# Optimization experiments

Hardware: AMD Instinct MI355X
Metric: run time of the kernel (lower is better)

Reference implementation:

```python
import jax, jax.numpy as jnp
import numpy as np

B, K = 16, 50
IN_CH, N_CLASSES, N_ANCH = 256, 80, 3
STRIDE, FSIZE, IGNORE_THRE = 8, 76, 0.7
N_CH = 5 + N_CLASSES
ANCHORS = np.array([[10,13],[16,30],[33,23],[30,61],[62,45],[59,119],[116,90],[156,198],[373,326]], np.float32)
ALL_GRID = ANCHORS / STRIDE            # all 9 anchors in grid units
ANCH_MASK = np.array([0, 1, 2])        # layer_no = 2
MASKED = ALL_GRID[ANCH_MASK]           # (3,2) anchors used by this head


def setup_inputs():
    key = jax.random.key(0)
    k1, k2, k3, k4, k5, k6 = jax.random.split(key, 6)
    xin = jax.random.normal(k1, (B, IN_CH, FSIZE, FSIZE), jnp.float32)
    cls = jax.random.randint(k2, (B, K), 0, N_CLASSES).astype(jnp.float32)
    xy = jax.random.uniform(k3, (B, K, 2), minval=0.05, maxval=0.95)
    wh = jax.random.uniform(k4, (B, K, 2), minval=0.02, maxval=0.30)
    labels = jnp.concatenate([cls[..., None], xy, wh], -1)   # (B,K,5) [cls,xc,yc,w,h]
    oc = N_ANCH * N_CH
    conv_w = jax.random.normal(k5, (oc, IN_CH), jnp.float32) * 0.01
    conv_b = jax.random.normal(k6, (oc,), jnp.float32) * 0.01
    return {"xin": xin, "labels": labels, "conv_w": conv_w, "conv_b": conv_b}


def _yolo(xin, conv_w, conv_b, labels):
    f, C = FSIZE, N_CLASSES
    # 1x1 conv == channel matmul
    raw = jnp.einsum('bchw,oc->bohw', xin, conv_w) + conv_b[None, :, None, None]
    raw = raw.reshape(B, N_ANCH, N_CH, f, f).transpose(0, 1, 3, 4, 2)  # (B,A,f,f,85)
    # sigmoid on x,y,obj,cls; w,h stay raw
    out = jnp.concatenate([jax.nn.sigmoid(raw[..., :2]), raw[..., 2:4], jax.nn.sigmoid(raw[..., 4:])], -1)

    grid = jnp.arange(f, dtype=jnp.float32)
    mw = jnp.asarray(MASKED[:, 0]); mh = jnp.asarray(MASKED[:, 1])
    px = out[..., 0] + grid[None, None, None, :]
    py = out[..., 1] + grid[None, None, :, None]
    pw = jnp.exp(out[..., 2]) * mw[None, :, None, None]
    ph = jnp.exp(out[..., 3]) * mh[None, :, None, None]
    pred = jax.lax.stop_gradient(jnp.stack([px, py, pw, ph], -1))  # detached, like torch .data

    labels = jax.lax.stop_gradient(labels)
    valid = labels.sum(-1) > 0                  # (B,K) padding rows are all-zero
    tx = labels[..., 1] * f; ty = labels[..., 2] * f
    tw = labels[..., 3] * f; th = labels[..., 4] * f
    ii = tx.astype(jnp.int32); jj = ty.astype(jnp.int32)

    # anchor matching: IoU of [0,0,w,h] truth vs [0,0,aw,ah] ref anchors (corners at origin)
    aw = jnp.asarray(ALL_GRID[:, 0]); ah = jnp.asarray(ALL_GRID[:, 1])
    inter_a = jnp.minimum(tw[..., None], aw) * jnp.minimum(th[..., None], ah)  # (B,K,9)
    iou_a = inter_a / (tw[..., None] * th[..., None] + aw * ah - inter_a)
    best_n_all = jnp.argmax(iou_a, -1)
    best_n = best_n_all % 3
    best_mask = (best_n_all == ANCH_MASK[0]) | (best_n_all == ANCH_MASK[1]) | (best_n_all == ANCH_MASK[2])

    # pred-vs-truth IoU in cxcywh form (xyxy=False)
    pa = pred.reshape(B, -1, 4)                 # (B, A*f*f, 4)
    tb = jnp.stack([tx, ty, tw, th], -1)        # (B, K, 4)
    tl = jnp.maximum(pa[:, :, None, :2] - pa[:, :, None, 2:] * 0.5, tb[:, None, :, :2] - tb[:, None, :, 2:] * 0.5)
    br = jnp.minimum(pa[:, :, None, :2] + pa[:, :, None, 2:] * 0.5, tb[:, None, :, :2] + tb[:, None, :, 2:] * 0.5)
    en = jnp.all(tl < br, -1)
    inter = jnp.prod(br - tl, -1) * en
    area_p = pa[..., 2] * pa[..., 3]; area_t = tb[..., 2] * tb[..., 3]
    iou_p = inter / (area_p[:, :, None] + area_t[:, None, :] - inter)
    iou_p = jnp.where(valid[:, None, :], iou_p, 0.0)
    ignore = (iou_p.max(-1) > IGNORE_THRE).reshape(B, N_ANCH, f, f)
    obj_mask = 1.0 - ignore.astype(jnp.float32)

    # scatter positive targets; non-selected rows routed out-of-bounds and dropped
    sel = valid & best_mask
    bb = jnp.where(sel, jnp.arange(B)[:, None], B)
    obj_mask = obj_mask.at[bb, best_n, jj, ii].set(1.0, mode='drop')
    tgt_mask = jnp.zeros((B, N_ANCH, f, f, 4 + C)).at[bb, best_n, jj, ii].set(1.0, mode='drop')
    scale = jnp.sqrt(2.0 - tw * th / (f * f))
    tgt_scale = jnp.zeros((B, N_ANCH, f, f, 2)).at[bb, best_n, jj, ii].set(
        jnp.broadcast_to(scale[..., None], (B, K, 2)), mode='drop')
    tvals = jnp.concatenate([
        (tx - ii)[..., None], (ty - jj)[..., None],
        jnp.log(tw / mw[best_n] + 1e-16)[..., None],
        jnp.log(th / mh[best_n] + 1e-16)[..., None],
        jnp.ones((B, K, 1), jnp.float32),
        jax.nn.one_hot(labels[..., 0].astype(jnp.int32), C)], -1)  # (B,K,85)
    target = jnp.zeros((B, N_ANCH, f, f, N_CH)).at[bb, best_n, jj, ii].set(tvals, mode='drop')

    oxy = out[..., :2] * tgt_mask[..., :2]
    owh = out[..., 2:4] * tgt_mask[..., 2:4] * tgt_scale
    oob = out[..., 4] * obj_mask
    ocl = out[..., 5:] * tgt_mask[..., 4:]
    txy = target[..., :2] * tgt_mask[..., :2]
    twh = target[..., 2:4] * tgt_mask[..., 2:4] * tgt_scale
    tob = target[..., 4] * obj_mask
    tcl = target[..., 5:] * tgt_mask[..., 4:]

    def bce(p, t, w=None):
        pc = jnp.clip(p, 1e-12, 1.0 - 1e-7)
        e = -(t * jnp.log(pc) + (1.0 - t) * jnp.log(1.0 - pc))
        if w is not None:
            e = e * w
        return e.sum()

    loss_xy = bce(oxy, txy, tgt_scale * tgt_scale)
    loss_wh = 0.5 * jnp.sum((owh - twh) ** 2)
    loss_obj = bce(oob, tob)
    loss_cls = bce(ocl, tcl)
    out_m = jnp.concatenate([oxy, owh, oob[..., None], ocl], -1)
    tgt_m = jnp.concatenate([txy, twh, tob[..., None], tcl], -1)
    loss_l2 = jnp.sum((out_m - tgt_m) ** 2)
    loss = loss_xy + loss_wh + loss_obj + loss_cls
    return loss, loss_xy, loss_wh, loss_obj, loss_cls, loss_l2, out_m


def reference(xin, labels, conv_w, conv_b):
    return _yolo(xin, conv_w, conv_b, labels)
```

## Files before the change

### kernel.cpp

```cpp
#include <hip/hip_runtime.h>
#include <hip/hip_bf16.h>

#define B_   16
#define K_   50
#define CIN  256
#define F_   76
#define A_   3
#define NCH  85
#define OC   255
#define HW   (F_*F_)
#define NBLK (B_*F_)
#define NCELL (A_*F_)
#define SLAB (F_*NCH)

#define WS_BIAS_F 32768
#define WS_LAB_F  33024
#define WS_PART_F 45824
#define WS_W15_F  55552
#define WS_XT_F   57600
#define XT_FLOATS (11829248u)

#define NTILE 91

typedef __attribute__((ext_vector_type(8))) short short8;
typedef __attribute__((ext_vector_type(4))) float f32x4;

__device__ __constant__ float AW9[9] = {1.25f, 2.0f, 4.125f, 3.75f, 7.75f, 7.375f, 14.5f, 19.5f, 46.625f};
__device__ __constant__ float AH9[9] = {1.625f, 3.75f, 2.875f, 7.625f, 5.625f, 14.875f, 11.25f, 24.75f, 40.75f};

__device__ __forceinline__ unsigned short f2bf(float f) {
    union { float f; unsigned int u; } v; v.f = f;
    unsigned int r = v.u + 0x7fffu + ((v.u >> 16) & 1u);
    return (unsigned short)(r >> 16);
}
__device__ __forceinline__ float bf2f(unsigned short b) {
    union { unsigned int u; float f; } v; v.u = ((unsigned int)b) << 16;
    return v.f;
}
__device__ __forceinline__ float sigm(float r) { return 1.0f / (1.0f + __expf(-r)); }
__device__ __forceinline__ float bce_t(float p, float tv) {
    float pc = fminf(fmaxf(p, 1e-12f), 1.0f - 1e-7f);
    return -(tv * __logf(pc) + (1.0f - tv) * __logf(1.0f - pc));
}

template<bool XTP>
__global__ void prep_kernel(const float* __restrict__ conv_w, const float* __restrict__ conv_b,
                            const float* __restrict__ labels, const float* __restrict__ xin,
                            float* __restrict__ ws) {
    __shared__ float tS[64][65];
    int bid = blockIdx.x, t = threadIdx.x;
    if (bid < 256) {
        float v = (t < OC) ? conv_w[t * CIN + bid] : 0.0f;
        ((unsigned short*)ws)[bid * 256 + t] = f2bf(v);
    } else if (bid == 256) {
        ws[WS_BIAS_F + t] = (t < OC) ? conv_b[t] : 0.0f;
    } else if (bid == 257) {
        for (int idx = t; idx < B_ * K_; idx += 256) {
            const float* L = labels + idx * 5;
            float cls = L[0], xc = L[1], yc = L[2], wl = L[3], hl = L[4];
            float ssum = cls + xc + yc + wl + hl;
            float validf = (ssum > 0.0f) ? 1.0f : 0.0f;
            float tx = xc * F_, ty = yc * F_, tw = wl * F_, th = hl * F_;
            int ii = (int)tx, jj = (int)ty;
            float tarea = tw * th;
            float best = -1.0f; int bn = 0;
            #pragma unroll
            for (int n = 0; n < 9; n++) {
                float inter = fminf(tw, AW9[n]) * fminf(th, AH9[n]);
                float iou = inter / (tarea + AW9[n] * AH9[n] - inter);
                if (iou > best) { best = iou; bn = n; }
            }
            int a = bn % 3;
            bool self = (validf != 0.0f) && (bn < 3);
            float* R = ws + WS_LAB_F + idx * 16;
            R[0] = tx; R[1] = ty; R[2] = tw; R[3] = th;
            R[4] = validf; R[5] = self ? (float)a : -1.0f; R[6] = (float)ii; R[7] = (float)jj;
            R[8] = tx - (float)ii; R[9] = ty - (float)jj;
            R[10] = __logf(tw / AW9[a] + 1e-16f);
            R[11] = __logf(th / AH9[a] + 1e-16f);
            R[12] = sqrtf(2.0f - tarea / (float)HW);
            R[13] = cls; R[14] = 0.0f; R[15] = 0.0f;
        }
    } else if (bid == 258) {
        unsigned short* wf = (unsigned short*)(ws + WS_W15_F);
        for (int idx = t; idx < 4096; idx += 256) {
            int ks = idx >> 9, lane = (idx >> 3) & 63, jj = idx & 7;
            int row = lane & 15;
            int k = ks * 32 + (lane >> 4) * 8 + jj;
            float v = 0.0f;
            if (row < 15) v = conv_w[((row / 5) * NCH + (row % 5)) * CIN + k];
            wf[idx] = f2bf(v);
        }
    } else if (XTP) {
        int bid2 = bid - 259;
        int bt = bid2 / NTILE, tile = bid2 - bt * NTILE;
        int hw0 = tile * 64;
        int npos = HW - hw0; if (npos > 64) npos = 64;
        unsigned short* xT = (unsigned short*)(ws + WS_XT_F);
        const float* xb = xin + (size_t)bt * CIN * HW + hw0;
        const int c_l = t >> 2, g = t & 3;
        for (int cc = 0; cc < 4; cc++) {
            const float* src = xb + (size_t)(cc * 64 + c_l) * HW;
            #pragma unroll
            for (int k2 = 0; k2 < 4; k2++) {
                int p_l = 4 * g + 16 * k2;
                if (p_l < npos) {
                    float4 v = *(const float4*)(src + p_l);
                    tS[c_l][p_l] = v.x; tS[c_l][p_l + 1] = v.y;
                    tS[c_l][p_l + 2] = v.z; tS[c_l][p_l + 3] = v.w;
                }
            }
            __syncthreads();
            if (c_l < npos) {
                unsigned int ow[8];
                #pragma unroll
                for (int u = 0; u < 8; u++) {
                    __hip_bfloat162 h = __float22bfloat162_rn(
                        make_float2(tS[g * 16 + 2 * u][c_l], tS[g * 16 + 2 * u + 1][c_l]));
                    ow[u] = *(unsigned int*)&h;
                }
                uint4* dst = (uint4*)(xT + ((size_t)bt * HW + hw0 + c_l) * 256 + cc * 64 + g * 16);
                dst[0] = make_uint4(ow[0], ow[1], ow[2], ow[3]);
                dst[1] = make_uint4(ow[4], ow[5], ow[6], ow[7]);
            }
            __syncthreads();
        }
    }
}

template<bool XT>
__global__ __launch_bounds__(320) void fused_kernel(const float* __restrict__ xin,
                                                    const float* __restrict__ ws,
                                                    float* __restrict__ d_out,
                                                    float* __restrict__ part) {
    __shared__ float raw5S[15 * F_];
    __shared__ float4 LAB[K_ * 4];
    __shared__ int   flagS[NCELL];
    __shared__ float omvS[NCELL];
    __shared__ float xcolS[256];
    __shared__ float redS[5][5];

    const int t = threadIdx.x;
    const int w = t >> 6, lane = t & 63;
    const int b = blockIdx.x / F_;
    const int j = blockIdx.x % F_;
    const int lr = lane & 15, q = lane >> 4;
    const int col0 = (w < 4) ? (w << 4) : 60;

    if (t < K_ * 4) LAB[t] = ((const float4*)(ws + WS_LAB_F + b * (K_ * 16)))[t];

    const unsigned short* wf15 = (const unsigned short*)(ws + WS_W15_F);
    short8 afr[8];
    #pragma unroll
    for (int ks = 0; ks < 8; ks++)
        afr[ks] = *(const short8*)&wf15[(ks * 64 + lane) * 8];

    f32x4 acc = (f32x4){0.0f, 0.0f, 0.0f, 0.0f};
    if (XT) {
        const unsigned short* xTp = (const unsigned short*)(ws + WS_XT_F)
                                  + ((size_t)(b * HW + j * F_ + col0 + lr)) * 256;
        #pragma unroll
        for (int ks = 0; ks < 8; ks++) {
            short8 bfr = *(const short8*)(xTp + ks * 32 + q * 8);
            acc = __builtin_amdgcn_mfma_f32_16x16x32_bf16(afr[ks], bfr, acc, 0, 0, 0);
        }
    } else {
        const float* xbase = xin + (size_t)b * CIN * HW + j * F_ + col0 + lr;
        #pragma unroll
        for (int ks = 0; ks < 8; ks++) {
            int kb = ks * 32 + q * 8;
            float xv[8];
            #pragma unroll
            for (int jj = 0; jj < 8; jj++) xv[jj] = xbase[(size_t)(kb + jj) * HW];
            union { short8 s; __hip_bfloat162 h[4]; } u;
            #pragma unroll
            for (int p = 0; p < 4; p++)
                u.h[p] = __float22bfloat162_rn(make_float2(xv[2 * p], xv[2 * p + 1]));
            acc = __builtin_amdgcn_mfma_f32_16x16x32_bf16(afr[ks], u.s, acc, 0, 0, 0);
        }
    }

    const float* biasg = ws + WS_BIAS_F;
    if (w < 4 || lr >= 4) {
        #pragma unroll
        for (int r = 0; r < 4; r++) {
            int row = q * 4 + r;
            if (row < 15) {
                int o = (row / 5) * NCH + (row % 5);
                raw5S[row * F_ + col0 + lr] = acc[r] + biasg[o];
            }
        }
    }
    __syncthreads();

    float lxy = 0.0f, lwh = 0.0f, lobj = 0.0f, lcls = 0.0f, l2 = 0.0f;
    if (t < NCELL) {
        int a = t / F_, i = t - a * F_;
        float x   = sigm(raw5S[(a * 5 + 0) * F_ + i]);
        float y   = sigm(raw5S[(a * 5 + 1) * F_ + i]);
        float wr  = raw5S[(a * 5 + 2) * F_ + i];
        float hr  = raw5S[(a * 5 + 3) * F_ + i];
        float obj = sigm(raw5S[(a * 5 + 4) * F_ + i]);

        float px = x + (float)i, py = y + (float)j;
        float pw = __expf(wr) * AW9[a], ph = __expf(hr) * AH9[a];
        float hpw = pw * 0.5f, hph = ph * 0.5f;
        float areap = pw * ph;
        float fa_t = (float)a, fi_t = (float)i, fj_t = (float)j;

        float maxiou = 0.0f; int mk = -1;
        #pragma unroll 2
        for (int k = 0; k < K_; k++) {
            float4 A0 = LAB[4 * k + 0];
            float4 A1 = LAB[4 * k + 1];
            float tx = A0.x, ty = A0.y, tw = A0.z, th = A0.w;
            float tlx = fmaxf(px - hpw, tx - tw * 0.5f);
            float tly = fmaxf(py - hph, ty - th * 0.5f);
            float brx = fminf(px + hpw, tx + tw * 0.5f);
            float bry = fminf(py + hph, ty + th * 0.5f);
            float iw = brx - tlx, ih = bry - tly;
            float inter = (iw > 0.0f && ih > 0.0f) ? iw * ih : 0.0f;
            float iou = __fdividef(inter, areap + tw * th - inter);
            iou = (A1.x != 0.0f) ? iou : 0.0f;
            maxiou = fmaxf(maxiou, iou);
            bool match = (A1.y == fa_t) & (A1.z == fi_t) & (A1.w == fj_t);
            mk = match ? k : mk;
        }
        float objmask = (maxiou > 0.7f) ? 0.0f : 1.0f;

        if (mk >= 0) {
            float4 B0 = LAB[4 * mk + 2];
            float4 B1 = LAB[4 * mk + 3];
            float sc = B1.x, sc2 = sc * sc;
            float txv = B0.x, tyv = B0.y, twv = B0.z, thv = B0.w;
            lxy = (bce_t(x, txv) + bce_t(y, tyv)) * sc2;
            float dw = wr - twv, dh = hr - thv;
            lwh = 0.5f * sc2 * (dw * dw + dh * dh);
            float pco = fminf(fmaxf(obj, 1e-12f), 1.0f - 1e-7f);
            lobj = -__logf(pco);
            float dx = x - txv, dy = y - tyv, dob = obj - 1.0f;
            l2 = dx * dx + dy * dy + sc2 * (dw * dw + dh * dh) + dob * dob;
            flagS[t] = mk + 1;
            omvS[t]  = obj;
        } else {
            float oo = obj * objmask;
            if (objmask != 0.0f) {
                float pco = fminf(obj, 1.0f - 1e-7f);
                lobj = -__logf(1.0f - pco);
            }
            l2 = oo * oo;
            flagS[t] = 0;
            omvS[t]  = oo;
        }
    }
    __syncthreads();

    #pragma unroll
    for (int a = 0; a < A_; a++) {
        float* slab = d_out + 6 + (size_t)((b * A_ + a) * F_ + j) * SLAB;
        const float* om = &omvS[a * F_];
        if (t == 0) { slab[0] = 0.0f; slab[1] = 0.0f; }
        if (t == 1) { slab[6458] = 0.0f; slab[6459] = 0.0f; }
        float4* dst4 = (float4*)(slab + 2);
        for (int n = t; n < 1614; n += 320) {
            int f0 = 2 + 4 * n;
            int p = f0 / 85, r = f0 - 85 * p;
            float4 v = make_float4(0.0f, 0.0f, 0.0f, 0.0f);
            if (r >= 1 && r <= 4) ((float*)&v)[4 - r] = om[p];
            dst4[n] = v;
        }
    }
    __syncthreads();

    const unsigned short* Wtg = (const unsigned short*)ws;
    for (int k = 0; k < K_; k++) {
        float4 A1 = LAB[4 * k + 1];
        int fa = (int)A1.y;
        if (fa < 0) continue;
        if ((int)A1.w != j) continue;
        int fi = (int)A1.z;
        int cell = fa * F_ + fi;
        if (flagS[cell] != k + 1) continue;

        if (t < 256) xcolS[t] = xin[((size_t)b * CIN + t) * HW + j * F_ + fi];
        __syncthreads();
        float4 B1 = LAB[4 * k + 3];
        float sc = B1.x; int cl = (int)B1.y;
        if (t < NCH) {
            float v; int chout;
            if (t < 80) {
                int o = fa * NCH + 5 + t;
                float accv = biasg[o];
                #pragma unroll 8
                for (int kk = 0; kk < 256; kk++)
                    accv += bf2f(Wtg[kk * 256 + o]) * xcolS[kk];
                float p = sigm(accv);
                float tcv = (t == cl) ? 1.0f : 0.0f;
                lcls += bce_t(p, tcv);
                float d = p - tcv;
                l2 += d * d;
                v = p; chout = 5 + t;
            } else {
                int ch = t - 80;
                float raw = raw5S[(fa * 5 + ch) * F_ + fi];
                v = (ch == 2 || ch == 3) ? raw * sc : sigm(raw);
                chout = ch;
            }
            d_out[6 + (size_t)((b * A_ + fa) * F_ + j) * SLAB + fi * NCH + chout] = v;
        }
        __syncthreads();
    }

    #pragma unroll
    for (int off = 32; off > 0; off >>= 1) {
        lxy  += __shfl_down(lxy, off);
        lwh  += __shfl_down(lwh, off);
        lobj += __shfl_down(lobj, off);
        lcls += __shfl_down(lcls, off);
        l2   += __shfl_down(l2, off);
    }
    if (lane == 0) {
        redS[w][0] = lxy; redS[w][1] = lwh; redS[w][2] = lobj;
        redS[w][3] = lcls; redS[w][4] = l2;
    }
    __syncthreads();
    if (t == 0) {
        float* P = part + (size_t)blockIdx.x * 8;
        #pragma unroll
        for (int q2 = 0; q2 < 5; q2++)
            P[q2] = redS[0][q2] + redS[1][q2] + redS[2][q2] + redS[3][q2] + redS[4][q2];
    }
}

__global__ void finish_kernel(const float* __restrict__ part, float* __restrict__ d_out) {
    int t = threadIdx.x;
    float s0 = 0, s1 = 0, s2 = 0, s3 = 0, s4 = 0;
    for (int bidx = t; bidx < NBLK; bidx += 256) {
        const float* P = part + (size_t)bidx * 8;
        s0 += P[0]; s1 += P[1]; s2 += P[2]; s3 += P[3]; s4 += P[4];
    }
    #pragma unroll
    for (int off = 32; off > 0; off >>= 1) {
        s0 += __shfl_down(s0, off); s1 += __shfl_down(s1, off);
        s2 += __shfl_down(s2, off); s3 += __shfl_down(s3, off);
        s4 += __shfl_down(s4, off);
    }
    __shared__ float red[4][5];
    if ((t & 63) == 0) {
        int w = t >> 6;
        red[w][0] = s0; red[w][1] = s1; red[w][2] = s2; red[w][3] = s3; red[w][4] = s4;
    }
    __syncthreads();
    if (t == 0) {
        float r0 = red[0][0] + red[1][0] + red[2][0] + red[3][0];
        float r1 = red[0][1] + red[1][1] + red[2][1] + red[3][1];
        float r2 = red[0][2] + red[1][2] + red[2][2] + red[3][2];
        float r3 = red[0][3] + red[1][3] + red[2][3] + red[3][3];
        float r4 = red[0][4] + red[1][4] + red[2][4] + red[3][4];
        d_out[0] = r0 + r1 + r2 + r3;
        d_out[1] = r0; d_out[2] = r1; d_out[3] = r2; d_out[4] = r3; d_out[5] = r4;
    }
}

extern "C" void kernel_launch(void* const* d_in, const int* in_sizes, int n_in,
                              void* d_out, int out_size, void* d_ws, size_t ws_size,
                              hipStream_t stream) {
    const float* xin    = (const float*)d_in[0];
    const float* labels = (const float*)d_in[1];
    const float* conv_w = (const float*)d_in[2];
    const float* conv_b = (const float*)d_in[3];
    float* out  = (float*)d_out;
    float* ws   = (float*)d_ws;
    float* part = ws + WS_PART_F;

    const size_t need = ((size_t)WS_XT_F + (size_t)XT_FLOATS) * 4u;
    if (ws_size >= need) {
        prep_kernel<true><<<259 + B_ * NTILE, 256, 0, stream>>>(conv_w, conv_b, labels, xin, ws);
        fused_kernel<true><<<NBLK, 320, 0, stream>>>(xin, ws, out, part);
    } else {
        prep_kernel<false><<<259, 256, 0, stream>>>(conv_w, conv_b, labels, xin, ws);
        fused_kernel<false><<<NBLK, 320, 0, stream>>>(xin, ws, out, part);
    }
    finish_kernel<<<1, 256, 0, stream>>>(part, out);
}
```

Measured before the change: 224.8 us.

## Compute 15-row conv in tiled kernel and stage raw outputs instead of bf16 transpose

Drops the pass that wrote a full bf16 transposed copy of the input (about 47MB round trip) to the workspace. A separate conv kernel now reads input tiles into shared memory with coalesced float4 loads and runs MFMA on the 15 needed rows. It writes only a small 15xHW fp32 raw buffer, which the fused kernel loads in place of doing its own matmul. This cuts global traffic sharply, at the cost of an extra kernel launch and a serialization point between the conv and prep kernels.

```diff
diff --git a/kernel.cpp b/kernel.cpp
--- a/kernel.cpp
+++ b/kernel.cpp
@@ -17,8 +17,8 @@
 #define WS_LAB_F  33024
 #define WS_PART_F 45824
 #define WS_W15_F  55552
-#define WS_XT_F   57600
-#define XT_FLOATS (11829248u)
+#define WS_RAW5_F 57600
+#define RAW5_FLOATS (B_*15*HW)
 
 #define NTILE 91
 
@@ -43,11 +43,8 @@
     return -(tv * __logf(pc) + (1.0f - tv) * __logf(1.0f - pc));
 }
 
-template<bool XTP>
 __global__ void prep_kernel(const float* __restrict__ conv_w, const float* __restrict__ conv_b,
-                            const float* __restrict__ labels, const float* __restrict__ xin,
-                            float* __restrict__ ws) {
-    __shared__ float tS[64][65];
+                            const float* __restrict__ labels, float* __restrict__ ws) {
     int bid = blockIdx.x, t = threadIdx.x;
     if (bid < 256) {
         float v = (t < OC) ? conv_w[t * CIN + bid] : 0.0f;
@@ -81,7 +78,7 @@
             R[12] = sqrtf(2.0f - tarea / (float)HW);
             R[13] = cls; R[14] = 0.0f; R[15] = 0.0f;
         }
-    } else if (bid == 258) {
+    } else {
         unsigned short* wf = (unsigned short*)(ws + WS_W15_F);
         for (int idx = t; idx < 4096; idx += 256) {
             int ks = idx >> 9, lane = (idx >> 3) & 63, jj = idx & 7;
@@ -91,44 +88,71 @@
             if (row < 15) v = conv_w[((row / 5) * NCH + (row % 5)) * CIN + k];
             wf[idx] = f2bf(v);
         }
-    } else if (XTP) {
-        int bid2 = bid - 259;
-        int bt = bid2 / NTILE, tile = bid2 - bt * NTILE;
-        int hw0 = tile * 64;
-        int npos = HW - hw0; if (npos > 64) npos = 64;
-        unsigned short* xT = (unsigned short*)(ws + WS_XT_F);
-        const float* xb = xin + (size_t)bt * CIN * HW + hw0;
-        const int c_l = t >> 2, g = t & 3;
-        for (int cc = 0; cc < 4; cc++) {
-            const float* src = xb + (size_t)(cc * 64 + c_l) * HW;
-            #pragma unroll
-            for (int k2 = 0; k2 < 4; k2++) {
-                int p_l = 4 * g + 16 * k2;
-                if (p_l < npos) {
-                    float4 v = *(const float4*)(src + p_l);
-                    tS[c_l][p_l] = v.x; tS[c_l][p_l + 1] = v.y;
-                    tS[c_l][p_l + 2] = v.z; tS[c_l][p_l + 3] = v.w;
-                }
-            }
-            __syncthreads();
-            if (c_l < npos) {
-                unsigned int ow[8];
-                #pragma unroll
-                for (int u = 0; u < 8; u++) {
-                    __hip_bfloat162 h = __float22bfloat162_rn(
-                        make_float2(tS[g * 16 + 2 * u][c_l], tS[g * 16 + 2 * u + 1][c_l]));
-                    ow[u] = *(unsigned int*)&h;
-                }
-                uint4* dst = (uint4*)(xT + ((size_t)bt * HW + hw0 + c_l) * 256 + cc * 64 + g * 16);
-                dst[0] = make_uint4(ow[0], ow[1], ow[2], ow[3]);
-                dst[1] = make_uint4(ow[4], ow[5], ow[6], ow[7]);
-            }
-            __syncthreads();
-        }
-    }
-}
-
-template<bool XT>
+    }
+}
+
+__global__ __launch_bounds__(256) void conv_kernel(const float* __restrict__ xin,
+                                                   const float* __restrict__ ws,
+                                                   float* __restrict__ raw5g) {
+    __shared__ float tS[64][65];
+    const int t = threadIdx.x;
+    const int w = t >> 6, lane = t & 63;
+    const int lr = lane & 15, q = lane >> 4;
+    const int bt = blockIdx.x / NTILE, tile = blockIdx.x - bt * NTILE;
+    const int hw0 = tile * 64;
+    const int npos = (HW - hw0 < 64) ? (HW - hw0) : 64;
+
+    const unsigned short* wf15 = (const unsigned short*)(ws + WS_W15_F);
+    short8 afr[8];
+    #pragma unroll
+    for (int ks = 0; ks < 8; ks++)
+        afr[ks] = *(const short8*)&wf15[(ks * 64 + lane) * 8];
+
+    f32x4 acc = (f32x4){0.0f, 0.0f, 0.0f, 0.0f};
+    const float* xb = xin + (size_t)bt * CIN * HW + hw0;
+    const int c_l = t >> 2, g = t & 3;
+    #pragma unroll 1
+    for (int cc = 0; cc < 4; cc++) {
+        const float* src = xb + (size_t)(cc * 64 + c_l) * HW;
+        #pragma unroll
+        for (int k2 = 0; k2 < 4; k2++) {
+            int p_l = 4 * g + 16 * k2;
+            if (p_l < npos) {
+                float4 v = *(const float4*)(src + p_l);
+                tS[c_l][p_l] = v.x; tS[c_l][p_l + 1] = v.y;
+                tS[c_l][p_l + 2] = v.z; tS[c_l][p_l + 3] = v.w;
+            }
+        }
+        __syncthreads();
+        #pragma unroll
+        for (int m = 0; m < 2; m++) {
+            float xv[8];
+            #pragma unroll
+            for (int jj = 0; jj < 8; jj++)
+                xv[jj] = tS[m * 32 + q * 8 + jj][w * 16 + lr];
+            union { short8 s; __hip_bfloat162 h[4]; } u;
+            #pragma unroll
+            for (int p2 = 0; p2 < 4; p2++)
+                u.h[p2] = __float22bfloat162_rn(make_float2(xv[2 * p2], xv[2 * p2 + 1]));
+            acc = __builtin_amdgcn_mfma_f32_16x16x32_bf16(afr[cc * 2 + m], u.s, acc, 0, 0, 0);
+        }
+        __syncthreads();
+    }
+    const float* biasg = ws + WS_BIAS_F;
+    const int p = w * 16 + lr;
+    if (hw0 + p < HW) {
+        #pragma unroll
+        for (int r = 0; r < 4; r++) {
+            int row = q * 4 + r;
+            if (row < 15) {
+                int o = (row / 5) * NCH + (row % 5);
+                raw5g[((size_t)bt * 15 + row) * HW + hw0 + p] = acc[r] + biasg[o];
+            }
+        }
+    }
+}
+
+template<bool R5>
 __global__ __launch_bounds__(320) void fused_kernel(const float* __restrict__ xin,
                                                     const float* __restrict__ ws,
                                                     float* __restrict__ d_out,
@@ -144,27 +168,25 @@
     const int w = t >> 6, lane = t & 63;
     const int b = blockIdx.x / F_;
     const int j = blockIdx.x % F_;
-    const int lr = lane & 15, q = lane >> 4;
-    const int col0 = (w < 4) ? (w << 4) : 60;
 
     if (t < K_ * 4) LAB[t] = ((const float4*)(ws + WS_LAB_F + b * (K_ * 16)))[t];
-
-    const unsigned short* wf15 = (const unsigned short*)(ws + WS_W15_F);
-    short8 afr[8];
-    #pragma unroll
-    for (int ks = 0; ks < 8; ks++)
-        afr[ks] = *(const short8*)&wf15[(ks * 64 + lane) * 8];
-
-    f32x4 acc = (f32x4){0.0f, 0.0f, 0.0f, 0.0f};
-    if (XT) {
-        const unsigned short* xTp = (const unsigned short*)(ws + WS_XT_F)
-                                  + ((size_t)(b * HW + j * F_ + col0 + lr)) * 256;
-        #pragma unroll
-        for (int ks = 0; ks < 8; ks++) {
-            short8 bfr = *(const short8*)(xTp + ks * 32 + q * 8);
-            acc = __builtin_amdgcn_mfma_f32_16x16x32_bf16(afr[ks], bfr, acc, 0, 0, 0);
+    const float* biasg = ws + WS_BIAS_F;
+
+    if (R5) {
+        const float* r5 = ws + WS_RAW5_F + (size_t)b * 15 * HW + j * F_;
+        for (int idx = t; idx < 15 * F_; idx += 320) {
+            int row = idx / F_, i = idx - row * F_;
+            raw5S[idx] = r5[row * HW + i];
         }
     } else {
+        const int lr = lane & 15, q = lane >> 4;
+        const int col0 = (w < 4) ? (w << 4) : 60;
+        const unsigned short* wf15 = (const unsigned short*)(ws + WS_W15_F);
+        short8 afr[8];
+        #pragma unroll
+        for (int ks = 0; ks < 8; ks++)
+            afr[ks] = *(const short8*)&wf15[(ks * 64 + lane) * 8];
+        f32x4 acc = (f32x4){0.0f, 0.0f, 0.0f, 0.0f};
         const float* xbase = xin + (size_t)b * CIN * HW + j * F_ + col0 + lr;
         #pragma unroll
         for (int ks = 0; ks < 8; ks++) {
@@ -178,16 +200,14 @@
                 u.h[p] = __float22bfloat162_rn(make_float2(xv[2 * p], xv[2 * p + 1]));
             acc = __builtin_amdgcn_mfma_f32_16x16x32_bf16(afr[ks], u.s, acc, 0, 0, 0);
         }
-    }
-
-    const float* biasg = ws + WS_BIAS_F;
-    if (w < 4 || lr >= 4) {
-        #pragma unroll
-        for (int r = 0; r < 4; r++) {
-            int row = q * 4 + r;
-            if (row < 15) {
-                int o = (row / 5) * NCH + (row % 5);
-                raw5S[row * F_ + col0 + lr] = acc[r] + biasg[o];
+        if (w < 4 || lr >= 4) {
+            #pragma unroll
+            for (int r = 0; r < 4; r++) {
+                int row = q * 4 + r;
+                if (row < 15) {
+                    int o = (row / 5) * NCH + (row % 5);
+                    raw5S[row * F_ + col0 + lr] = acc[r] + biasg[o];
+                }
             }
         }
     }
@@ -373,12 +393,12 @@
     float* ws   = (float*)d_ws;
     float* part = ws + WS_PART_F;
 
-    const size_t need = ((size_t)WS_XT_F + (size_t)XT_FLOATS) * 4u;
+    prep_kernel<<<259, 256, 0, stream>>>(conv_w, conv_b, labels, ws);
+    const size_t need = ((size_t)WS_RAW5_F + (size_t)RAW5_FLOATS) * 4u;
     if (ws_size >= need) {
-        prep_kernel<true><<<259 + B_ * NTILE, 256, 0, stream>>>(conv_w, conv_b, labels, xin, ws);
+        conv_kernel<<<B_ * NTILE, 256, 0, stream>>>(xin, ws, ws + WS_RAW5_F);
         fused_kernel<true><<<NBLK, 320, 0, stream>>>(xin, ws, out, part);
     } else {
-        prep_kernel<false><<<259, 256, 0, stream>>>(conv_w, conv_b, labels, xin, ws);
         fused_kernel<false><<<NBLK, 320, 0, stream>>>(xin, ws, out, part);
     }
     finish_kernel<<<1, 256, 0, stream>>>(part, out);
```

Result: slower. 285.3 us (+26.9%).
